# Kernel tuning notes

Measured on AMD Instinct MI355X. Metric: run time of the kernel, lower is better.

Reference implementation:

```python
import jax, jax.numpy as jnp
import numpy as np

C = 256
HEADS = 4
RADIUS = 2
LN_EPS = 1e-5


def setup_inputs() -> dict:
    key = jax.random.key(0)
    ks = jax.random.split(key, 8)
    s = 0.02
    return {
        "feat": jax.random.normal(ks[0], (8, C, 64, 64), dtype=jnp.float32),
        "in_w": jax.random.normal(ks[1], (3 * C, C), dtype=jnp.float32) * s,
        "in_b": jnp.zeros((3 * C,), dtype=jnp.float32),
        "out_w": jax.random.normal(ks[2], (C, C), dtype=jnp.float32) * s,
        "out_b": jnp.zeros((C,), dtype=jnp.float32),
        "proj_w": jax.random.normal(ks[3], (C, 4 * C), dtype=jnp.float32) * s,
        "proj_b": jnp.zeros((C,), dtype=jnp.float32),
        "ln_g": jnp.ones((C,), dtype=jnp.float32),
        "ln_b": jnp.zeros((C,), dtype=jnp.float32),
    }


def _spatial_mask(h, w, radius):
    yy, xx = jnp.meshgrid(jnp.arange(h), jnp.arange(w), indexing="ij")
    coords = jnp.stack([yy.ravel(), xx.ravel()], axis=-1).astype(jnp.float32)  # [N,2]
    dist = jnp.abs(coords[:, None, :] - coords[None, :, :]).sum(-1)  # Manhattan [N,N]
    return jnp.where(dist > radius, -jnp.inf, 0.0).astype(jnp.float32)


def _attend(qf, mf, mask, in_w, in_b, out_w, out_b, proj_w, proj_b, ln_g, ln_b):
    b, c, h, w = qf.shape
    n = h * w
    d = c // HEADS
    qt = qf.reshape(b, c, n).transpose(0, 2, 1)  # [B,N,C]
    mt = mf.reshape(b, c, n).transpose(0, 2, 1)
    q = qt @ in_w[:c].T + in_b[:c]
    k = mt @ in_w[c:2 * c].T + in_b[c:2 * c]
    v = mt @ in_w[2 * c:].T + in_b[2 * c:]
    # [B,H,N,D]
    q = q.reshape(b, n, HEADS, d).transpose(0, 2, 1, 3)
    k = k.reshape(b, n, HEADS, d).transpose(0, 2, 1, 3)
    v = v.reshape(b, n, HEADS, d).transpose(0, 2, 1, 3)
    scores = jnp.einsum("bhnd,bhmd->bhnm", q, k) / jnp.sqrt(jnp.float32(d)) + mask
    attn = jax.nn.softmax(scores, axis=-1)
    ctx = jnp.einsum("bhnm,bhmd->bhnd", attn, v)
    ctx = ctx.transpose(0, 2, 1, 3).reshape(b, n, c) @ out_w.T + out_b  # [B,N,C]
    asym = jnp.concatenate([qt, ctx, jnp.abs(qt - ctx), qt * ctx], axis=-1)
    y = asym @ proj_w.T + proj_b
    mu = y.mean(-1, keepdims=True)
    var = ((y - mu) ** 2).mean(-1, keepdims=True)
    y = (y - mu) / jnp.sqrt(var + LN_EPS) * ln_g + ln_b
    y = jax.nn.relu(y)
    return y.transpose(0, 2, 1).reshape(b, c, h, w)


def reference(feat, in_w, in_b, out_w, out_b, proj_w, proj_b, ln_g, ln_b):
    b, c, h, w = feat.shape
    mid = w // 2
    left = feat[:, :, :, :mid]
    right = feat[:, :, :, mid:]
    right_mirror = right[:, :, :, ::-1]
    left_mirror = left[:, :, :, ::-1]
    mask = _spatial_mask(h, mid, RADIUS)
    args = (mask, in_w, in_b, out_w, out_b, proj_w, proj_b, ln_g, ln_b)
    left_asym = _attend(left, right_mirror, *args)
    right_asym = _attend(right, left_mirror, *args)
    return jnp.concatenate([left_asym, right_asym], axis=-1)
```

## Files before the change

kernel.cpp:

```cpp
#include <hip/hip_runtime.h>
#include <hip/hip_bf16.h>


#define NTOK 32768

using bf16x8 = __attribute__((ext_vector_type(8))) short;
using f32x4  = __attribute__((ext_vector_type(4))) float;

__device__ __forceinline__ float b2f(short s) {
    unsigned u = ((unsigned)(unsigned short)s) << 16;
    union { unsigned u; float f; } c; c.u = u; return c.f;
}
__device__ __forceinline__ short f2b(float f) {
    __hip_bfloat16 h = __float2bfloat16(f);
    return *(short*)&h;
}
__device__ __forceinline__ void async_copy16(const void* g, void* l) {
    __builtin_amdgcn_global_load_lds(
        (const __attribute__((address_space(1))) unsigned int*)g,
        (__attribute__((address_space(3))) unsigned int*)l, 16, 0, 0);
}

__global__ __launch_bounds__(256) void prep_kernel(const float* __restrict__ feat,
                                                   const float* __restrict__ in_w,
                                                   const float* __restrict__ out_w,
                                                   const float* __restrict__ proj_w,
                                                   __hip_bfloat16* __restrict__ X,
                                                   __hip_bfloat16* __restrict__ wbf) {
    const int bid = blockIdx.x;
    const int tid = threadIdx.x;
    if (bid < 4096) {
        __shared__ float tile[32][68];
        const int b   = bid >> 9;
        const int rem = bid & 511;
        const int sp0 = (rem & 63) * 64;
        const int c0  = (rem >> 6) * 32;
        #pragma unroll
        for (int u = 0; u < 2; ++u) {
            const int idx = tid + u * 256;
            const int cl = idx >> 4;
            const int sq = (idx & 15) * 4;
            const float4 v = *(const float4*)(feat + ((size_t)(b * 256 + c0 + cl) << 12) + sp0 + sq);
            tile[cl][sq]     = v.x;
            tile[cl][sq + 1] = v.y;
            tile[cl][sq + 2] = v.z;
            tile[cl][sq + 3] = v.w;
        }
        __syncthreads();
        #pragma unroll
        for (int u = 0; u < 2; ++u) {
            const int idx = tid + u * 256;
            const int tok = idx >> 3;
            const int cq  = (idx & 7) * 4;
            short4 s;
            s.x = f2b(tile[cq][tok]);
            s.y = f2b(tile[cq + 1][tok]);
            s.z = f2b(tile[cq + 2][tok]);
            s.w = f2b(tile[cq + 3][tok]);
            *(short4*)(X + (size_t)(b * 4096 + sp0 + tok) * 256 + c0 + cq) = s;
        }
    } else {
        const int i4 = (bid - 4096) * 1024 + tid * 4;
        if (i4 < 196608) {
            const float4 v = *(const float4*)(in_w + i4);
            short4 s = {f2b(v.x), f2b(v.y), f2b(v.z), f2b(v.w)};
            *(short4*)(wbf + i4) = s;
        }
        if (i4 < 65536) {
            const float4 v = *(const float4*)(out_w + i4);
            short4 s = {f2b(v.x), f2b(v.y), f2b(v.z), f2b(v.w)};
            *(short4*)(wbf + 196608 + i4) = s;
        }
        if (i4 < 262144) {
            const float4 v = *(const float4*)(proj_w + i4);
            short4 s = {f2b(v.x), f2b(v.y), f2b(v.z), f2b(v.w)};
            *(short4*)(wbf + 262144 + i4) = s;
        }
    }
}

template <int KDIM, bool OUT_BF16>
__global__ __launch_bounds__(256) void mfma_gemm(const __hip_bfloat16* __restrict__ A,
                                                 const __hip_bfloat16* __restrict__ W,
                                                 const float* __restrict__ bias,
                                                 void* __restrict__ C, int Ntot) {
    __shared__ __align__(16) short As[2][128 * 64];
    __shared__ __align__(16) short Bs[2][128 * 64];
    const int tid = threadIdx.x;
    const int work = (blockIdx.x & 7) * 192 + (blockIdx.x >> 3);
    const int m0 = (work / 6) * 128;
    const int n0 = (work % 6) * 128;
    const int wave = tid >> 6, lane = tid & 63;
    const int wm = (wave >> 1) * 64;
    const int wn = (wave & 1) * 64;
    const int fm = lane & 15;
    const int fq = lane >> 4;

    #pragma unroll
    for (int v = 0; v < 4; ++v) {
        const int qb = v * 256 + wave * 64;
        const int q = qb + lane;
        const int r = q >> 3;
        const int cs = (q & 7) ^ (r & 7);
        async_copy16(A + (size_t)(m0 + r) * KDIM + cs * 8, &As[0][qb * 8]);
        async_copy16(W + (size_t)(n0 + r) * KDIM + cs * 8, &Bs[0][qb * 8]);
    }
    __syncthreads();

    f32x4 acc[4][4] = {};
    #pragma unroll
    for (int t = 0; t < KDIM / 64; ++t) {
        const int cur = t & 1;
        if (t + 1 < KDIM / 64) {
            #pragma unroll
            for (int v = 0; v < 4; ++v) {
                const int qb = v * 256 + wave * 64;
                const int q = qb + lane;
                const int r = q >> 3;
                const int cs = (q & 7) ^ (r & 7);
                async_copy16(A + (size_t)(m0 + r) * KDIM + (t + 1) * 64 + cs * 8, &As[cur ^ 1][qb * 8]);
                async_copy16(W + (size_t)(n0 + r) * KDIM + (t + 1) * 64 + cs * 8, &Bs[cur ^ 1][qb * 8]);
            }
        }
        #pragma unroll
        for (int kk = 0; kk < 2; ++kk) {
            bf16x8 af[4], bw[4];
            #pragma unroll
            for (int i = 0; i < 4; ++i) {
                const int row = wm + i * 16 + fm;
                af[i] = *(const bf16x8*)(&As[cur][row * 64 + (((fq + kk * 4) ^ (fm & 7)) * 8)]);
            }
            #pragma unroll
            for (int j = 0; j < 4; ++j) {
                const int row = wn + j * 16 + fm;
                bw[j] = *(const bf16x8*)(&Bs[cur][row * 64 + (((fq + kk * 4) ^ (fm & 7)) * 8)]);
            }
            #pragma unroll
            for (int i = 0; i < 4; ++i)
                #pragma unroll
                for (int j = 0; j < 4; ++j)
                    acc[i][j] = __builtin_amdgcn_mfma_f32_16x16x32_bf16(af[i], bw[j], acc[i][j], 0, 0, 0);
        }
        __syncthreads();
    }
    #pragma unroll
    for (int j = 0; j < 4; ++j) {
        const int col = n0 + wn + j * 16 + fm;
        const float bv = bias[col];
        #pragma unroll
        for (int i = 0; i < 4; ++i) {
            #pragma unroll
            for (int r = 0; r < 4; ++r) {
                const int row = m0 + wm + i * 16 + fq * 4 + r;
                const float v = acc[i][j][r] + bv;
                if (OUT_BF16)
                    ((__hip_bfloat16*)C)[(size_t)row * Ntot + col] = __float2bfloat16(v);
                else
                    ((float*)C)[(size_t)row * Ntot + col] = v;
            }
        }
    }
}

#define P0DY ((2u)|(2u<<3)|(2u<<6)|(2u<<9)|(2u<<12)|(1u<<15)|(1u<<18)|(1u<<21))
#define P0DX ((2u)|(1u<<3)|(3u<<6)|(0u<<9)|(4u<<12)|(2u<<15)|(1u<<18)|(3u<<21))
#define P1DY ((3u)|(3u<<3)|(3u<<6)|(0u<<9)|(4u<<12)|(2u<<15)|(2u<<18)|(2u<<21))
#define P1DX ((2u)|(1u<<3)|(3u<<6)|(2u<<9)|(2u<<12)|(2u<<15)|(2u<<18)|(2u<<21))

__global__ __launch_bounds__(256) void attn_kernel(const __hip_bfloat16* __restrict__ qkv,
                                                   __hip_bfloat16* __restrict__ ctx) {
    const int t = blockIdx.x * 4 + (threadIdx.x >> 6);
    const int lane = threadIdx.x & 63;
    const int n  = lane >> 3;
    const int cg = lane & 7;
    const int x6 = t & 63;
    const int yq = (t >> 6) & 63;
    const int b  = t >> 12;
    const int side = x6 >> 5;
    const int x = x6 & 31;

    bool valid[2];
    size_t kb[2];
    #pragma unroll
    for (int p = 0; p < 2; ++p) {
        const unsigned dyp = p ? P1DY : P0DY;
        const unsigned dxp = p ? P1DX : P0DX;
        const int sh = 3 * n;
        const int dy = (int)((dyp >> sh) & 7) - 2;
        const int dx = (int)((dxp >> sh) & 7) - 2;
        const int yy = yq + dy, xx = x + dx;
        valid[p] = (p == 0 || n < 5) && yy >= 0 && yy < 64 && xx >= 0 && xx < 32;
        const int xm = side ? (31 - xx) : (63 - xx);
        int tm = (b << 12) + (yy << 6) + xm;
        if (!valid[p]) tm = t;
        kb[p] = (size_t)tm * 768 + 256 + cg * 8;
    }
    const size_t qb = (size_t)t * 768 + cg * 8;
    const size_t ob = (size_t)t * 256;

    #pragma unroll
    for (int hp = 0; hp < 2; ++hp) {
        bf16x8 q8[2], k8[2][2], v8[2][2];
        #pragma unroll
        for (int hh = 0; hh < 2; ++hh) {
            const int h = hp * 2 + hh;
            q8[hh] = *(const bf16x8*)(qkv + qb + h * 64);
            #pragma unroll
            for (int p = 0; p < 2; ++p) {
                k8[hh][p] = *(const bf16x8*)(qkv + kb[p] + h * 64);
                v8[hh][p] = *(const bf16x8*)(qkv + kb[p] + h * 64 + 256);
            }
        }
        #pragma unroll
        for (int hh = 0; hh < 2; ++hh) {
            float sc[2];
            #pragma unroll
            for (int p = 0; p < 2; ++p) {
                float s = 0.f;
                #pragma unroll
                for (int j = 0; j < 8; ++j) s += b2f(q8[hh][j]) * b2f(k8[hh][p][j]);
                s += __shfl_xor(s, 1, 64);
                s += __shfl_xor(s, 2, 64);
                s += __shfl_xor(s, 4, 64);
                sc[p] = valid[p] ? s * 0.125f : -1e30f;
            }
            const float p0 = __expf(sc[0]);
            const float p1 = __expf(sc[1]);
            float l = p0 + p1;
            l += __shfl_xor(l, 8, 64);
            l += __shfl_xor(l, 16, 64);
            l += __shfl_xor(l, 32, 64);

            float o[8];
            #pragma unroll
            for (int j = 0; j < 8; ++j)
                o[j] = p0 * b2f(v8[hh][0][j]) + p1 * b2f(v8[hh][1][j]);
            float r4[4];
            #pragma unroll
            for (int i = 0; i < 4; ++i) {
                const float a = o[2 * i], bb = o[2 * i + 1];
                const float mine = (n & 1) ? bb : a;
                const float theirs = (n & 1) ? a : bb;
                r4[i] = mine + __shfl_xor(theirs, 8, 64);
            }
            float r2[2];
            #pragma unroll
            for (int i = 0; i < 2; ++i) {
                const float a = r4[2 * i], bb = r4[2 * i + 1];
                const float mine = (n & 2) ? bb : a;
                const float theirs = (n & 2) ? a : bb;
                r2[i] = mine + __shfl_xor(theirs, 16, 64);
            }
            float ov;
            {
                const float a = r2[0], bb = r2[1];
                const float mine = (n & 4) ? bb : a;
                const float theirs = (n & 4) ? a : bb;
                ov = mine + __shfl_xor(theirs, 32, 64);
            }
            const float rl = __builtin_amdgcn_rcpf(l);
            ctx[ob + (hp * 2 + hh) * 64 + cg * 8 + n] = __float2bfloat16(ov * rl);
        }
    }
}

__global__ __launch_bounds__(512, 4) void proj_ln_fused(const __hip_bfloat16* __restrict__ X,
                                                        const __hip_bfloat16* __restrict__ CTX,
                                                        const __hip_bfloat16* __restrict__ W2,
                                                        const float* __restrict__ out_b,
                                                        const __hip_bfloat16* __restrict__ W,
                                                        const float* __restrict__ bias,
                                                        const float* __restrict__ ln_g,
                                                        const float* __restrict__ ln_b,
                                                        float* __restrict__ out) {
    __shared__ __align__(16) short smem[36864];
    __shared__ float mu_s[64], inv_s[64];
    short* c2s = smem;
    short* As  = smem + 16384;
    short* Bs  = smem + 20480;
    const int tid = threadIdx.x;
    const int m0 = blockIdx.x * 64;
    const int b = m0 >> 12, sp0 = m0 & 4095;
    const int wave = tid >> 6, lane = tid & 63;
    const int wmh = (wave >> 2) * 32;
    const int wn  = (wave & 3) * 64;
    const int fm = lane & 15;
    const int fq = lane >> 4;

    {
        f32x4 acc2[2][4] = {};
        for (int k0 = 0; k0 < 256; k0 += 64) {
            {
                const int q = tid;
                const int r = q >> 3;
                const int cs = (q & 7) ^ (r & 7);
                async_copy16(CTX + (size_t)(m0 + r) * 256 + k0 + cs * 8, &As[(wave * 64) * 8]);
            }
            #pragma unroll
            for (int v = 0; v < 4; ++v) {
                const int q = v * 512 + tid;
                const int r = q >> 3;
                const int cs = (q & 7) ^ (r & 7);
                async_copy16(W2 + (size_t)r * 256 + k0 + cs * 8, &Bs[(v * 512 + wave * 64) * 8]);
            }
            __syncthreads();
            #pragma unroll
            for (int kk = 0; kk < 2; ++kk) {
                bf16x8 af[2], bw[4];
                #pragma unroll
                for (int i = 0; i < 2; ++i) {
                    const int row = wmh + i * 16 + fm;
                    af[i] = *(const bf16x8*)(&As[row * 64 + (((fq + kk * 4) ^ (fm & 7)) * 8)]);
                }
                #pragma unroll
                for (int j = 0; j < 4; ++j) {
                    const int row = wn + j * 16 + fm;
                    bw[j] = *(const bf16x8*)(&Bs[row * 64 + (((fq + kk * 4) ^ (fm & 7)) * 8)]);
                }
                #pragma unroll
                for (int i = 0; i < 2; ++i)
                    #pragma unroll
                    for (int j = 0; j < 4; ++j)
                        acc2[i][j] = __builtin_amdgcn_mfma_f32_16x16x32_bf16(af[i], bw[j], acc2[i][j], 0, 0, 0);
            }
            __syncthreads();
        }
        #pragma unroll
        for (int j = 0; j < 4; ++j) {
            const int col = wn + j * 16 + fm;
            const float bv = out_b[col];
            const int jch = col >> 3, cl = col & 7;
            #pragma unroll
            for (int i = 0; i < 2; ++i)
                #pragma unroll
                for (int rr = 0; rr < 4; ++rr) {
                    const int row = wmh + i * 16 + fq * 4 + rr;
                    const int slot = (jch & 24) | ((jch & 7) ^ (row & 7));
                    c2s[row * 256 + slot * 8 + cl] = f2b(acc2[i][j][rr] + bv);
                }
        }
    }
    __syncthreads();

    f32x4 acc[2][4] = {};
    for (int k0 = 0; k0 < 1024; k0 += 64) {
        const int g = k0 >> 8;
        const int cb = k0 & 255;
        #pragma unroll
        for (int v = 0; v < 4; ++v) {
            const int q = v * 512 + tid;
            const int r = q >> 3;
            const int cs = (q & 7) ^ (r & 7);
            async_copy16(W + (size_t)r * 1024 + k0 + cs * 8, &Bs[(v * 512 + wave * 64) * 8]);
        }
        if (g == 0) {
            const int q = tid;
            const int r = q >> 3;
            const int cs = (q & 7) ^ (r & 7);
            async_copy16(X + (size_t)(m0 + r) * 256 + cb + cs * 8, &As[(wave * 64) * 8]);
        } else if (g >= 2) {
            const int q = tid;
            const int r = q >> 3;
            const int cs = (q & 7) ^ (r & 7);
            int4 qraw = *(const int4*)(X + (size_t)(m0 + r) * 256 + cb + cs * 8);
            const int jch = (cb >> 3) + cs;
            const int slot = (jch & 24) | ((jch & 7) ^ (r & 7));
            int4 craw = *(const int4*)(&c2s[r * 256 + slot * 8]);
            const short* qs = (const short*)&qraw;
            const short* cw = (const short*)&craw;
            short tmp[8];
            #pragma unroll
            for (int j = 0; j < 8; ++j) {
                const float qv = b2f(qs[j]), cv = b2f(cw[j]);
                tmp[j] = f2b(g == 2 ? fabsf(qv - cv) : qv * cv);
            }
            *(int4*)(&As[q * 8]) = *(int4*)tmp;
        }
        __syncthreads();
        #pragma unroll
        for (int kk = 0; kk < 2; ++kk) {
            bf16x8 af[2], bw[4];
            if (g == 1) {
                #pragma unroll
                for (int i = 0; i < 2; ++i) {
                    const int row = wmh + i * 16 + fm;
                    const int jch = (cb >> 3) + fq + kk * 4;
                    const int slot = (jch & 24) | ((jch & 7) ^ (row & 7));
                    af[i] = *(const bf16x8*)(&c2s[row * 256 + slot * 8]);
                }
            } else {
                #pragma unroll
                for (int i = 0; i < 2; ++i) {
                    const int row = wmh + i * 16 + fm;
                    af[i] = *(const bf16x8*)(&As[row * 64 + (((fq + kk * 4) ^ (fm & 7)) * 8)]);
                }
            }
            #pragma unroll
            for (int j = 0; j < 4; ++j) {
                const int row = wn + j * 16 + fm;
                bw[j] = *(const bf16x8*)(&Bs[row * 64 + (((fq + kk * 4) ^ (fm & 7)) * 8)]);
            }
            #pragma unroll
            for (int i = 0; i < 2; ++i)
                #pragma unroll
                for (int j = 0; j < 4; ++j)
                    acc[i][j] = __builtin_amdgcn_mfma_f32_16x16x32_bf16(af[i], bw[j], acc[i][j], 0, 0, 0);
        }
        __syncthreads();
    }
    short* ys = smem;
    #pragma unroll
    for (int j = 0; j < 4; ++j) {
        const int col = wn + j * 16 + fm;
        const float bv = bias[col];
        #pragma unroll
        for (int i = 0; i < 2; ++i)
            #pragma unroll
            for (int r = 0; r < 4; ++r)
                ys[(wmh + i * 16 + fq * 4 + r) * 266 + col] = f2b(acc[i][j][r] + bv);
    }
    __syncthreads();
    {
        const int tt = tid >> 3, seg = tid & 7;
        float s = 0.f, ss = 0.f;
        #pragma unroll
        for (int j = 0; j < 32; ++j) {
            const float v = b2f(ys[tt * 266 + seg * 32 + j]);
            s += v; ss += v * v;
        }
        s += __shfl_xor(s, 1, 64);  ss += __shfl_xor(ss, 1, 64);
        s += __shfl_xor(s, 2, 64);  ss += __shfl_xor(ss, 2, 64);
        s += __shfl_xor(s, 4, 64);  ss += __shfl_xor(ss, 4, 64);
        if (seg == 0) {
            const float mu = s * (1.f / 256.f);
            const float var = ss * (1.f / 256.f) - mu * mu;
            mu_s[tt] = mu;
            inv_s[tt] = rsqrtf(var + 1e-5f);
        }
    }
    __syncthreads();
    {
        const int tl = tid & 63;
        const int j0 = tid >> 6;
        const float mu = mu_s[tl], inv = inv_s[tl];
        #pragma unroll
        for (int u = 0; u < 32; ++u) {
            const int j = j0 * 32 + u;
            const float v = (b2f(ys[tl * 266 + j]) - mu) * inv * ln_g[j] + ln_b[j];
            out[((size_t)(b * 256 + j) << 12) + sp0 + tl] = fmaxf(v, 0.f);
        }
    }
}

extern "C" void kernel_launch(void* const* d_in, const int* in_sizes, int n_in,
                              void* d_out, int out_size, void* d_ws, size_t ws_size,
                              hipStream_t stream) {
    (void)in_sizes; (void)n_in; (void)out_size; (void)ws_size;
    const float* feat   = (const float*)d_in[0];
    const float* in_w   = (const float*)d_in[1];
    const float* in_b   = (const float*)d_in[2];
    const float* out_w  = (const float*)d_in[3];
    const float* out_b  = (const float*)d_in[4];
    const float* proj_w = (const float*)d_in[5];
    const float* proj_b = (const float*)d_in[6];
    const float* ln_g   = (const float*)d_in[7];
    const float* ln_b   = (const float*)d_in[8];
    float* out = (float*)d_out;

    char* ws = (char*)d_ws;
    __hip_bfloat16* Xbf  = (__hip_bfloat16*)(ws);
    __hip_bfloat16* wbf  = (__hip_bfloat16*)(ws + (size_t)(16) * (1 << 20));
    __hip_bfloat16* qkv  = (__hip_bfloat16*)(ws + (size_t)(17) * (1 << 20));
    __hip_bfloat16* ctx  = (__hip_bfloat16*)(ws + (size_t)(65) * (1 << 20));
    __hip_bfloat16* in_wbf   = wbf;
    __hip_bfloat16* out_wbf  = wbf + 196608;
    __hip_bfloat16* proj_wbf = wbf + 262144;

    prep_kernel   <<<4352, 256, 0, stream>>>(feat, in_w, out_w, proj_w, Xbf, wbf);
    mfma_gemm<256, true><<<1536, 256, 0, stream>>>(Xbf, in_wbf, in_b, qkv, 768);
    attn_kernel   <<<NTOK / 4, 256, 0, stream>>>(qkv, ctx);
    proj_ln_fused <<<NTOK / 64, 512, 0, stream>>>(Xbf, ctx, out_wbf, out_b,
                                                  proj_wbf, proj_b, ln_g, ln_b, out);
}
```

Before: 180.8 us.

## Tile attention over 4x4 query blocks with K/V halo staged in LDS

The attention kernel now processes a 4x4 spatial tile of queries per block. It async-copies the 8x8 halo of mirrored K and V rows into XOR-swizzled shared memory, then reads neighbour keys from LDS instead of gathering them from global memory for every query. This removes redundant global K/V loads, since each neighbour row is shared by up to 13 queries. In exchange it uses 64KB of LDS per block, which limits occupancy, and each wave now loops serially over 4 queries.

```diff
diff --git a/kernel.cpp b/kernel.cpp
--- a/kernel.cpp
+++ b/kernel.cpp
@@ -169,97 +169,123 @@
 
 __global__ __launch_bounds__(256) void attn_kernel(const __hip_bfloat16* __restrict__ qkv,
                                                    __hip_bfloat16* __restrict__ ctx) {
-    const int t = blockIdx.x * 4 + (threadIdx.x >> 6);
-    const int lane = threadIdx.x & 63;
+    __shared__ __align__(16) short ks[16384];
+    __shared__ __align__(16) short vs[16384];
+    const int tid  = threadIdx.x;
+    const int wave = tid >> 6, lane = tid & 63;
+    const int bid  = blockIdx.x;
+    const int b    = bid >> 8;
+    const int rem  = bid & 255;
+    const int ty   = rem >> 4;
+    const int side = (rem >> 3) & 1;
+    const int tx   = rem & 7;
+    const int y0 = ty * 4, x0 = tx * 4;
+
+    #pragma unroll
+    for (int u = 0; u < 8; ++u) {
+        const int q = u * 256 + tid;
+        const int pos = q >> 5;
+        const int sl = q & 31;
+        const int gc = (sl & 24) | ((sl & 7) ^ (pos & 7));
+        const int yyl = pos >> 3, xxl = pos & 7;
+        int yy = y0 - 2 + yyl; yy = yy < 0 ? 0 : (yy > 63 ? 63 : yy);
+        int xx = x0 - 2 + xxl; xx = xx < 0 ? 0 : (xx > 31 ? 31 : xx);
+        const int xm = side ? (31 - xx) : (63 - xx);
+        const size_t tm = (size_t)((b << 12) + (yy << 6) + xm) * 768;
+        async_copy16(qkv + tm + 256 + gc * 8, &ks[(u * 256 + wave * 64) * 8]);
+        async_copy16(qkv + tm + 512 + gc * 8, &vs[(u * 256 + wave * 64) * 8]);
+    }
+    __syncthreads();
+
     const int n  = lane >> 3;
     const int cg = lane & 7;
-    const int x6 = t & 63;
-    const int yq = (t >> 6) & 63;
-    const int b  = t >> 12;
-    const int side = x6 >> 5;
-    const int x = x6 & 31;
-
-    bool valid[2];
-    size_t kb[2];
-    #pragma unroll
-    for (int p = 0; p < 2; ++p) {
-        const unsigned dyp = p ? P1DY : P0DY;
-        const unsigned dxp = p ? P1DX : P0DX;
-        const int sh = 3 * n;
-        const int dy = (int)((dyp >> sh) & 7) - 2;
-        const int dx = (int)((dxp >> sh) & 7) - 2;
-        const int yy = yq + dy, xx = x + dx;
-        valid[p] = (p == 0 || n < 5) && yy >= 0 && yy < 64 && xx >= 0 && xx < 32;
-        const int xm = side ? (31 - xx) : (63 - xx);
-        int tm = (b << 12) + (yy << 6) + xm;
-        if (!valid[p]) tm = t;
-        kb[p] = (size_t)tm * 768 + 256 + cg * 8;
-    }
-    const size_t qb = (size_t)t * 768 + cg * 8;
-    const size_t ob = (size_t)t * 256;
-
-    #pragma unroll
-    for (int hp = 0; hp < 2; ++hp) {
-        bf16x8 q8[2], k8[2][2], v8[2][2];
-        #pragma unroll
-        for (int hh = 0; hh < 2; ++hh) {
-            const int h = hp * 2 + hh;
-            q8[hh] = *(const bf16x8*)(qkv + qb + h * 64);
-            #pragma unroll
-            for (int p = 0; p < 2; ++p) {
-                k8[hh][p] = *(const bf16x8*)(qkv + kb[p] + h * 64);
-                v8[hh][p] = *(const bf16x8*)(qkv + kb[p] + h * 64 + 256);
-            }
-        }
-        #pragma unroll
-        for (int hh = 0; hh < 2; ++hh) {
-            float sc[2];
-            #pragma unroll
-            for (int p = 0; p < 2; ++p) {
-                float s = 0.f;
-                #pragma unroll
-                for (int j = 0; j < 8; ++j) s += b2f(q8[hh][j]) * b2f(k8[hh][p][j]);
-                s += __shfl_xor(s, 1, 64);
-                s += __shfl_xor(s, 2, 64);
-                s += __shfl_xor(s, 4, 64);
-                sc[p] = valid[p] ? s * 0.125f : -1e30f;
-            }
-            const float p0 = __expf(sc[0]);
-            const float p1 = __expf(sc[1]);
-            float l = p0 + p1;
-            l += __shfl_xor(l, 8, 64);
-            l += __shfl_xor(l, 16, 64);
-            l += __shfl_xor(l, 32, 64);
-
-            float o[8];
-            #pragma unroll
-            for (int j = 0; j < 8; ++j)
-                o[j] = p0 * b2f(v8[hh][0][j]) + p1 * b2f(v8[hh][1][j]);
-            float r4[4];
-            #pragma unroll
-            for (int i = 0; i < 4; ++i) {
-                const float a = o[2 * i], bb = o[2 * i + 1];
-                const float mine = (n & 1) ? bb : a;
-                const float theirs = (n & 1) ? a : bb;
-                r4[i] = mine + __shfl_xor(theirs, 8, 64);
-            }
-            float r2[2];
-            #pragma unroll
-            for (int i = 0; i < 2; ++i) {
-                const float a = r4[2 * i], bb = r4[2 * i + 1];
-                const float mine = (n & 2) ? bb : a;
-                const float theirs = (n & 2) ? a : bb;
-                r2[i] = mine + __shfl_xor(theirs, 16, 64);
-            }
-            float ov;
-            {
-                const float a = r2[0], bb = r2[1];
-                const float mine = (n & 4) ? bb : a;
-                const float theirs = (n & 4) ? a : bb;
-                ov = mine + __shfl_xor(theirs, 32, 64);
-            }
-            const float rl = __builtin_amdgcn_rcpf(l);
-            ctx[ob + (hp * 2 + hh) * 64 + cg * 8 + n] = __float2bfloat16(ov * rl);
+    const int y  = y0 + wave;
+    const int sh = 3 * n;
+    const int dy0 = (int)((P0DY >> sh) & 7) - 2;
+    const int dx0 = (int)((P0DX >> sh) & 7) - 2;
+    const int dy1 = (int)((P1DY >> sh) & 7) - 2;
+    const int dx1 = (int)((P1DX >> sh) & 7) - 2;
+
+    for (int xl = 0; xl < 4; ++xl) {
+        const int x = x0 + xl;
+        const int t = (b << 12) + (y << 6) + side * 32 + x;
+        bool valid[2];
+        int pos[2];
+        {
+            const int yyA = y + dy0, xxA = x + dx0;
+            valid[0] = yyA >= 0 && yyA < 64 && xxA >= 0 && xxA < 32;
+            pos[0] = (wave + dy0 + 2) * 8 + (xl + dx0 + 2);
+            const int yyB = y + dy1, xxB = x + dx1;
+            valid[1] = (n < 5) && yyB >= 0 && yyB < 64 && xxB >= 0 && xxB < 32;
+            pos[1] = (wave + dy1 + 2) * 8 + (xl + dx1 + 2);
+        }
+        const size_t qb = (size_t)t * 768 + cg * 8;
+        const size_t ob = (size_t)t * 256;
+
+        #pragma unroll
+        for (int hp = 0; hp < 2; ++hp) {
+            bf16x8 q8[2], k8[2][2], v8[2][2];
+            #pragma unroll
+            for (int hh = 0; hh < 2; ++hh) {
+                const int h = hp * 2 + hh;
+                q8[hh] = *(const bf16x8*)(qkv + qb + h * 64);
+                #pragma unroll
+                for (int p = 0; p < 2; ++p) {
+                    const int sl = h * 8 + (cg ^ (pos[p] & 7));
+                    k8[hh][p] = *(const bf16x8*)(&ks[pos[p] * 256 + sl * 8]);
+                    v8[hh][p] = *(const bf16x8*)(&vs[pos[p] * 256 + sl * 8]);
+                }
+            }
+            #pragma unroll
+            for (int hh = 0; hh < 2; ++hh) {
+                float sc[2];
+                #pragma unroll
+                for (int p = 0; p < 2; ++p) {
+                    float s = 0.f;
+                    #pragma unroll
+                    for (int j = 0; j < 8; ++j) s += b2f(q8[hh][j]) * b2f(k8[hh][p][j]);
+                    s += __shfl_xor(s, 1, 64);
+                    s += __shfl_xor(s, 2, 64);
+                    s += __shfl_xor(s, 4, 64);
+                    sc[p] = valid[p] ? s * 0.125f : -1e30f;
+                }
+                const float p0 = __expf(sc[0]);
+                const float p1 = __expf(sc[1]);
+                float l = p0 + p1;
+                l += __shfl_xor(l, 8, 64);
+                l += __shfl_xor(l, 16, 64);
+                l += __shfl_xor(l, 32, 64);
+
+                float o[8];
+                #pragma unroll
+                for (int j = 0; j < 8; ++j)
+                    o[j] = p0 * b2f(v8[hh][0][j]) + p1 * b2f(v8[hh][1][j]);
+                float r4[4];
+                #pragma unroll
+                for (int i = 0; i < 4; ++i) {
+                    const float a = o[2 * i], bb = o[2 * i + 1];
+                    const float mine = (n & 1) ? bb : a;
+                    const float theirs = (n & 1) ? a : bb;
+                    r4[i] = mine + __shfl_xor(theirs, 8, 64);
+                }
+                float r2[2];
+                #pragma unroll
+                for (int i = 0; i < 2; ++i) {
+                    const float a = r4[2 * i], bb = r4[2 * i + 1];
+                    const float mine = (n & 2) ? bb : a;
+                    const float theirs = (n & 2) ? a : bb;
+                    r2[i] = mine + __shfl_xor(theirs, 16, 64);
+                }
+                float ov;
+                {
+                    const float a = r2[0], bb = r2[1];
+                    const float mine = (n & 4) ? bb : a;
+                    const float theirs = (n & 4) ? a : bb;
+                    ov = mine + __shfl_xor(theirs, 32, 64);
+                }
+                const float rl = __builtin_amdgcn_rcpf(l);
+                ctx[ob + (hp * 2 + hh) * 64 + cg * 8 + n] = __float2bfloat16(ov * rl);
+            }
         }
     }
 }
@@ -478,7 +504,7 @@
 
     prep_kernel   <<<4352, 256, 0, stream>>>(feat, in_w, out_w, proj_w, Xbf, wbf);
     mfma_gemm<256, true><<<1536, 256, 0, stream>>>(Xbf, in_wbf, in_b, qkv, 768);
-    attn_kernel   <<<NTOK / 4, 256, 0, stream>>>(qkv, ctx);
+    attn_kernel   <<<2048, 256, 0, stream>>>(qkv, ctx);
     proj_ln_fused <<<NTOK / 64, 512, 0, stream>>>(Xbf, ctx, out_wbf, out_b,
                                                   proj_wbf, proj_b, ln_g, ln_b, out);
 }
```

New measurement: 202.5 us. 1.12x slower.
